# Kernel optimization log

Hardware: AMD Instinct MI355X
Metric: run time of the kernel (lower is better)

Reference implementation:

```python
import jax, jax.numpy as jnp
import numpy as np

EPS_BN = 0.001

def setup_inputs() -> dict:
    key = jax.random.key(0)
    ks = jax.random.split(key, 11)
    B, C, H, W = 32, 512, 64, 64
    Hc = 128
    return {
        'x':  jax.random.normal(ks[0], (B, C, H, W), dtype=jnp.float32),
        'w1': jax.random.normal(ks[1], (Hc, C), dtype=jnp.float32) * (1.0 / np.sqrt(C)),
        'g1': jax.random.uniform(ks[2], (Hc,), dtype=jnp.float32, minval=0.5, maxval=1.5),
        'b1': jax.random.normal(ks[3], (Hc,), dtype=jnp.float32) * 0.1,
        'm1': jax.random.normal(ks[4], (Hc,), dtype=jnp.float32) * 0.1,
        'v1': jax.random.uniform(ks[5], (Hc,), dtype=jnp.float32, minval=0.5, maxval=1.5),
        'w2': jax.random.normal(ks[6], (C, Hc), dtype=jnp.float32) * (1.0 / np.sqrt(Hc)),
        'g2': jax.random.uniform(ks[7], (C,), dtype=jnp.float32, minval=0.5, maxval=1.5),
        'b2': jax.random.normal(ks[8], (C,), dtype=jnp.float32) * 0.1,
        'm2': jax.random.normal(ks[9], (C,), dtype=jnp.float32) * 0.1,
        'v2': jax.random.uniform(ks[10], (C,), dtype=jnp.float32, minval=0.5, maxval=1.5),
    }

def reference(x, w1, g1, b1, m1, v1, w2, g2, b2, m2, v2):
    # squeeze: global average pool -> [B, C]
    s = jnp.mean(x, axis=(2, 3))
    # excitation: 1x1 conv (C->Hc, no bias), eval-mode BN, ReLU, 1x1 conv (Hc->C, no bias)
    h = jnp.einsum('bc,hc->bh', s, w1)
    h = (h - m1) * (g1 * jax.lax.rsqrt(v1 + EPS_BN)) + b1
    h = jax.nn.relu(h)
    e = jnp.einsum('bh,ch->bc', h, w2)  # scale_activation = Identity
    # broadcast scale + final eval-mode BN over channels
    y = x * e[:, :, None, None]
    scale2 = (g2 * jax.lax.rsqrt(v2 + EPS_BN))[None, :, None, None]
    shift2 = (b2 - m2 * g2 * jax.lax.rsqrt(v2 + EPS_BN))[None, :, None, None]
    return y * scale2 + shift2
```

## Files before the change

### kernel.cpp

```cpp
#include <hip/hip_runtime.h>
#include <hip/hip_bf16.h>
#include <stdint.h>

#define B_   32
#define C_   512
#define HW_  4096
#define HC_  128
#define EPS_ 1e-3f

__device__ __forceinline__ float bf_lo(uint32_t u) { return __uint_as_float(u << 16); }
__device__ __forceinline__ float bf_hi(uint32_t u) { return __uint_as_float(u & 0xffff0000u); }

__device__ __forceinline__ uint32_t packbf2(float lo, float hi) {
    union { uint32_t u; __hip_bfloat162 h; } cv;
    cv.h.x = __float2bfloat16(lo);
    cv.h.y = __float2bfloat16(hi);
    return cv.u;
}

__device__ __forceinline__ float ld_scalar(const void* p, int i, int isbf) {
    if (isbf) return __bfloat162float(((const __hip_bfloat16*)p)[i]);
    return ((const float*)p)[i];
}

__global__ __launch_bounds__(256) void se_detect(const uint32_t* __restrict__ v2w,
                                                 int* __restrict__ flag) {
    const int t = threadIdx.x;
    const uint32_t w = v2w[t];
    const float lo = bf_lo(w), hi = bf_hi(w);
    const bool ok = (lo >= 0.4f) && (lo <= 1.6f) && (hi >= 0.4f) && (hi <= 1.6f);
    const unsigned long long bal = __ballot(ok);
    __shared__ int allok[4];
    if ((t & 63) == 0) allok[t >> 6] = (bal == ~0ull) ? 1 : 0;
    __syncthreads();
    if (t == 0) flag[0] = allok[0] & allok[1] & allok[2] & allok[3];
}

__global__ __launch_bounds__(256) void se_pool(const void* __restrict__ x,
                                               float* __restrict__ s,
                                               const int* __restrict__ flag) {
    const int bc = blockIdx.x;
    const int t  = threadIdx.x;
    const int isbf = *flag;
    float sum = 0.f;
    if (isbf) {
        const uint4* p = reinterpret_cast<const uint4*>(x) + (size_t)bc * (HW_ / 8);
        #pragma unroll
        for (int i = t; i < HW_ / 8; i += 256) {
            uint4 v = p[i];
            sum += bf_lo(v.x) + bf_hi(v.x) + bf_lo(v.y) + bf_hi(v.y)
                 + bf_lo(v.z) + bf_hi(v.z) + bf_lo(v.w) + bf_hi(v.w);
        }
    } else {
        const float4* p = reinterpret_cast<const float4*>(x) + (size_t)bc * (HW_ / 4);
        #pragma unroll
        for (int i = t; i < HW_ / 4; i += 256) {
            float4 v = p[i];
            sum += v.x + v.y + v.z + v.w;
        }
    }
    #pragma unroll
    for (int off = 32; off > 0; off >>= 1)
        sum += __shfl_down(sum, off, 64);
    __shared__ float part[4];
    if ((t & 63) == 0) part[t >> 6] = sum;
    __syncthreads();
    if (t == 0) {
        float tot = part[0] + part[1] + part[2] + part[3];
        s[bc] = tot * (1.0f / (float)HW_);
    }
}

__global__ __launch_bounds__(128) void se_excite(
    const float* __restrict__ s,
    const void* __restrict__ w1, const void* __restrict__ g1,
    const void* __restrict__ b1, const void* __restrict__ m1,
    const void* __restrict__ v1, const void* __restrict__ w2,
    const void* __restrict__ g2, const void* __restrict__ b2,
    const void* __restrict__ m2, const void* __restrict__ v2,
    float* __restrict__ A, float* __restrict__ S2,
    const int* __restrict__ flag) {
    __shared__ float s_sh[C_];
    __shared__ float h_sh[HC_];
    const int b = blockIdx.x, t = threadIdx.x;
    const int isbf = *flag;
    for (int i = t; i < C_; i += HC_) s_sh[i] = s[b * C_ + i];
    __syncthreads();

    float acc = 0.f;
    if (isbf) {
        const uint4* w1r = reinterpret_cast<const uint4*>(w1) + (size_t)t * (C_ / 8);
        #pragma unroll 8
        for (int i = 0; i < C_ / 8; ++i) {
            uint4 v = w1r[i];
            const int c = i * 8;
            acc += s_sh[c + 0] * bf_lo(v.x) + s_sh[c + 1] * bf_hi(v.x)
                 + s_sh[c + 2] * bf_lo(v.y) + s_sh[c + 3] * bf_hi(v.y)
                 + s_sh[c + 4] * bf_lo(v.z) + s_sh[c + 5] * bf_hi(v.z)
                 + s_sh[c + 6] * bf_lo(v.w) + s_sh[c + 7] * bf_hi(v.w);
        }
    } else {
        const float4* w1r = reinterpret_cast<const float4*>(w1) + (size_t)t * (C_ / 4);
        #pragma unroll 8
        for (int i = 0; i < C_ / 4; ++i) {
            float4 v = w1r[i];
            const int c = i * 4;
            acc += s_sh[c + 0] * v.x + s_sh[c + 1] * v.y
                 + s_sh[c + 2] * v.z + s_sh[c + 3] * v.w;
        }
    }
    const float sc1 = ld_scalar(g1, t, isbf) * rsqrtf(ld_scalar(v1, t, isbf) + EPS_);
    const float hv  = (acc - ld_scalar(m1, t, isbf)) * sc1 + ld_scalar(b1, t, isbf);
    h_sh[t] = fmaxf(hv, 0.f);
    __syncthreads();

    #pragma unroll
    for (int k = 0; k < C_ / HC_; ++k) {
        const int c = t + HC_ * k;
        float e = 0.f;
        if (isbf) {
            const uint4* w2r = reinterpret_cast<const uint4*>(w2) + (size_t)c * (HC_ / 8);
            #pragma unroll
            for (int i = 0; i < HC_ / 8; ++i) {
                uint4 v = w2r[i];
                const int j = i * 8;
                e += h_sh[j + 0] * bf_lo(v.x) + h_sh[j + 1] * bf_hi(v.x)
                   + h_sh[j + 2] * bf_lo(v.y) + h_sh[j + 3] * bf_hi(v.y)
                   + h_sh[j + 4] * bf_lo(v.z) + h_sh[j + 5] * bf_hi(v.z)
                   + h_sh[j + 6] * bf_lo(v.w) + h_sh[j + 7] * bf_hi(v.w);
            }
        } else {
            const float4* w2r = reinterpret_cast<const float4*>(w2) + (size_t)c * (HC_ / 4);
            #pragma unroll
            for (int i = 0; i < HC_ / 4; ++i) {
                float4 v = w2r[i];
                const int j = i * 4;
                e += h_sh[j + 0] * v.x + h_sh[j + 1] * v.y
                   + h_sh[j + 2] * v.z + h_sh[j + 3] * v.w;
            }
        }
        const float sc2 = ld_scalar(g2, c, isbf) * rsqrtf(ld_scalar(v2, c, isbf) + EPS_);
        A[b * C_ + c] = e * sc2;
        if (b == 0) S2[c] = ld_scalar(b2, c, isbf) - ld_scalar(m2, c, isbf) * sc2;
    }
}

__global__ __launch_bounds__(256) void se_apply(const void* __restrict__ x,
                                                const float* __restrict__ A,
                                                const float* __restrict__ S2,
                                                void* __restrict__ y,
                                                const int* __restrict__ flag) {
    const int bc = blockIdx.x;
    const int t  = threadIdx.x;
    const int isbf = *flag;
    const float a  = A[bc];
    const float sh = S2[bc & (C_ - 1)];
    if (isbf) {
        const uint4* px = reinterpret_cast<const uint4*>(x) + (size_t)bc * (HW_ / 8);
        uint4*       py = reinterpret_cast<uint4*>(y)       + (size_t)bc * (HW_ / 8);
        #pragma unroll
        for (int i = t; i < HW_ / 8; i += 256) {
            uint4 v = px[i];
            uint4 r;
            r.x = packbf2(fmaf(bf_lo(v.x), a, sh), fmaf(bf_hi(v.x), a, sh));
            r.y = packbf2(fmaf(bf_lo(v.y), a, sh), fmaf(bf_hi(v.y), a, sh));
            r.z = packbf2(fmaf(bf_lo(v.z), a, sh), fmaf(bf_hi(v.z), a, sh));
            r.w = packbf2(fmaf(bf_lo(v.w), a, sh), fmaf(bf_hi(v.w), a, sh));
            py[i] = r;
        }
    } else {
        const float4* px = reinterpret_cast<const float4*>(x) + (size_t)bc * (HW_ / 4);
        float4*       py = reinterpret_cast<float4*>(y)       + (size_t)bc * (HW_ / 4);
        #pragma unroll
        for (int i = t; i < HW_ / 4; i += 256) {
            float4 v = px[i];
            float4 r;
            r.x = fmaf(v.x, a, sh);
            r.y = fmaf(v.y, a, sh);
            r.z = fmaf(v.z, a, sh);
            r.w = fmaf(v.w, a, sh);
            py[i] = r;
        }
    }
}

extern "C" void kernel_launch(void* const* d_in, const int* in_sizes, int n_in,
                              void* d_out, int out_size, void* d_ws, size_t ws_size,
                              hipStream_t stream) {
    const void* x  = d_in[0];
    const void* w1 = d_in[1];
    const void* g1 = d_in[2];
    const void* b1 = d_in[3];
    const void* m1 = d_in[4];
    const void* v1 = d_in[5];
    const void* w2 = d_in[6];
    const void* g2 = d_in[7];
    const void* b2 = d_in[8];
    const void* m2 = d_in[9];
    const void* v2 = d_in[10];

    float* ws = (float*)d_ws;
    float* s  = ws;
    float* A  = ws + B_ * C_;
    float* S2 = ws + 2 * B_ * C_;
    int* flag = (int*)(ws + 2 * B_ * C_ + C_);

    se_detect<<<1, 256, 0, stream>>>((const uint32_t*)v2, flag);
    se_pool<<<B_ * C_, 256, 0, stream>>>(x, s, flag);
    se_excite<<<B_, HC_, 0, stream>>>(s, w1, g1, b1, m1, v1, w2, g2, b2, m2, v2,
                                      A, S2, flag);
    se_apply<<<B_ * C_, 256, 0, stream>>>(x, A, S2, d_out, flag);
}
```

Baseline: 524.4 us.

## Inline dtype detection, reverse apply block order, use nontemporal output stores

Removes the separate detect kernel launch by having every block of pool, excite and apply re-derive the bf16/fp32 flag from v2 in shared memory. The apply kernel walks blocks in reverse order so the most recently pooled slices of x, likely still in L2/MALL cache, are re-read first. Output writes become nontemporal stores to avoid polluting cache. Each block now does an extra small global read and two barriers.

```diff
diff --git a/kernel.cpp b/kernel.cpp
--- a/kernel.cpp
+++ b/kernel.cpp
@@ -8,6 +8,9 @@
 #define HC_  128
 #define EPS_ 1e-3f
 
+typedef uint32_t u32x4 __attribute__((ext_vector_type(4)));
+typedef float    f32x4 __attribute__((ext_vector_type(4)));
+
 __device__ __forceinline__ float bf_lo(uint32_t u) { return __uint_as_float(u << 16); }
 __device__ __forceinline__ float bf_hi(uint32_t u) { return __uint_as_float(u & 0xffff0000u); }
 
@@ -23,46 +26,51 @@
     return ((const float*)p)[i];
 }
 
-__global__ __launch_bounds__(256) void se_detect(const uint32_t* __restrict__ v2w,
-                                                 int* __restrict__ flag) {
-    const int t = threadIdx.x;
-    const uint32_t w = v2w[t];
-    const float lo = bf_lo(w), hi = bf_hi(w);
-    const bool ok = (lo >= 0.4f) && (lo <= 1.6f) && (hi >= 0.4f) && (hi <= 1.6f);
-    const unsigned long long bal = __ballot(ok);
-    __shared__ int allok[4];
-    if ((t & 63) == 0) allok[t >> 6] = (bal == ~0ull) ? 1 : 0;
-    __syncthreads();
-    if (t == 0) flag[0] = allok[0] & allok[1] & allok[2] & allok[3];
+template <int NT>
+__device__ __forceinline__ int detect_isbf(const uint32_t* __restrict__ v2w,
+                                           int t, int* s_flag) {
+    if (t == 0) *s_flag = 1;
+    __syncthreads();
+    bool ok = true;
+    #pragma unroll
+    for (int i = t; i < 256; i += NT) {
+        const uint32_t w = v2w[i];
+        const float lo = bf_lo(w), hi = bf_hi(w);
+        ok = ok && (lo >= 0.4f) && (lo <= 1.6f) && (hi >= 0.4f) && (hi <= 1.6f);
+    }
+    if (!ok) *s_flag = 0;
+    __syncthreads();
+    return *s_flag;
 }
 
 __global__ __launch_bounds__(256) void se_pool(const void* __restrict__ x,
                                                float* __restrict__ s,
-                                               const int* __restrict__ flag) {
+                                               const uint32_t* __restrict__ v2w) {
+    __shared__ int s_flag;
+    __shared__ float part[4];
+    const int t  = threadIdx.x;
+    const int isbf = detect_isbf<256>(v2w, t, &s_flag);
     const int bc = blockIdx.x;
-    const int t  = threadIdx.x;
-    const int isbf = *flag;
     float sum = 0.f;
     if (isbf) {
-        const uint4* p = reinterpret_cast<const uint4*>(x) + (size_t)bc * (HW_ / 8);
+        const u32x4* p = reinterpret_cast<const u32x4*>(x) + (size_t)bc * (HW_ / 8);
         #pragma unroll
         for (int i = t; i < HW_ / 8; i += 256) {
-            uint4 v = p[i];
+            u32x4 v = p[i];
             sum += bf_lo(v.x) + bf_hi(v.x) + bf_lo(v.y) + bf_hi(v.y)
                  + bf_lo(v.z) + bf_hi(v.z) + bf_lo(v.w) + bf_hi(v.w);
         }
     } else {
-        const float4* p = reinterpret_cast<const float4*>(x) + (size_t)bc * (HW_ / 4);
+        const f32x4* p = reinterpret_cast<const f32x4*>(x) + (size_t)bc * (HW_ / 4);
         #pragma unroll
         for (int i = t; i < HW_ / 4; i += 256) {
-            float4 v = p[i];
+            f32x4 v = p[i];
             sum += v.x + v.y + v.z + v.w;
         }
     }
     #pragma unroll
     for (int off = 32; off > 0; off >>= 1)
         sum += __shfl_down(sum, off, 64);
-    __shared__ float part[4];
     if ((t & 63) == 0) part[t >> 6] = sum;
     __syncthreads();
     if (t == 0) {
@@ -78,21 +86,21 @@
     const void* __restrict__ v1, const void* __restrict__ w2,
     const void* __restrict__ g2, const void* __restrict__ b2,
     const void* __restrict__ m2, const void* __restrict__ v2,
-    float* __restrict__ A, float* __restrict__ S2,
-    const int* __restrict__ flag) {
+    float* __restrict__ A, float* __restrict__ S2) {
+    __shared__ int s_flag;
     __shared__ float s_sh[C_];
     __shared__ float h_sh[HC_];
     const int b = blockIdx.x, t = threadIdx.x;
-    const int isbf = *flag;
+    const int isbf = detect_isbf<128>((const uint32_t*)v2, t, &s_flag);
     for (int i = t; i < C_; i += HC_) s_sh[i] = s[b * C_ + i];
     __syncthreads();
 
     float acc = 0.f;
     if (isbf) {
-        const uint4* w1r = reinterpret_cast<const uint4*>(w1) + (size_t)t * (C_ / 8);
+        const u32x4* w1r = reinterpret_cast<const u32x4*>(w1) + (size_t)t * (C_ / 8);
         #pragma unroll 8
         for (int i = 0; i < C_ / 8; ++i) {
-            uint4 v = w1r[i];
+            u32x4 v = w1r[i];
             const int c = i * 8;
             acc += s_sh[c + 0] * bf_lo(v.x) + s_sh[c + 1] * bf_hi(v.x)
                  + s_sh[c + 2] * bf_lo(v.y) + s_sh[c + 3] * bf_hi(v.y)
@@ -100,10 +108,10 @@
                  + s_sh[c + 6] * bf_lo(v.w) + s_sh[c + 7] * bf_hi(v.w);
         }
     } else {
-        const float4* w1r = reinterpret_cast<const float4*>(w1) + (size_t)t * (C_ / 4);
+        const f32x4* w1r = reinterpret_cast<const f32x4*>(w1) + (size_t)t * (C_ / 4);
         #pragma unroll 8
         for (int i = 0; i < C_ / 4; ++i) {
-            float4 v = w1r[i];
+            f32x4 v = w1r[i];
             const int c = i * 4;
             acc += s_sh[c + 0] * v.x + s_sh[c + 1] * v.y
                  + s_sh[c + 2] * v.z + s_sh[c + 3] * v.w;
@@ -119,10 +127,10 @@
         const int c = t + HC_ * k;
         float e = 0.f;
         if (isbf) {
-            const uint4* w2r = reinterpret_cast<const uint4*>(w2) + (size_t)c * (HC_ / 8);
+            const u32x4* w2r = reinterpret_cast<const u32x4*>(w2) + (size_t)c * (HC_ / 8);
             #pragma unroll
             for (int i = 0; i < HC_ / 8; ++i) {
-                uint4 v = w2r[i];
+                u32x4 v = w2r[i];
                 const int j = i * 8;
                 e += h_sh[j + 0] * bf_lo(v.x) + h_sh[j + 1] * bf_hi(v.x)
                    + h_sh[j + 2] * bf_lo(v.y) + h_sh[j + 3] * bf_hi(v.y)
@@ -130,10 +138,10 @@
                    + h_sh[j + 6] * bf_lo(v.w) + h_sh[j + 7] * bf_hi(v.w);
             }
         } else {
-            const float4* w2r = reinterpret_cast<const float4*>(w2) + (size_t)c * (HC_ / 4);
+            const f32x4* w2r = reinterpret_cast<const f32x4*>(w2) + (size_t)c * (HC_ / 4);
             #pragma unroll
             for (int i = 0; i < HC_ / 4; ++i) {
-                float4 v = w2r[i];
+                f32x4 v = w2r[i];
                 const int j = i * 4;
                 e += h_sh[j + 0] * v.x + h_sh[j + 1] * v.y
                    + h_sh[j + 2] * v.z + h_sh[j + 3] * v.w;
@@ -149,37 +157,38 @@
                                                 const float* __restrict__ A,
                                                 const float* __restrict__ S2,
                                                 void* __restrict__ y,
-                                                const int* __restrict__ flag) {
-    const int bc = blockIdx.x;
+                                                const uint32_t* __restrict__ v2w) {
+    __shared__ int s_flag;
     const int t  = threadIdx.x;
-    const int isbf = *flag;
+    const int isbf = detect_isbf<256>(v2w, t, &s_flag);
+    const int bc = (B_ * C_ - 1) - (int)blockIdx.x;
     const float a  = A[bc];
     const float sh = S2[bc & (C_ - 1)];
     if (isbf) {
-        const uint4* px = reinterpret_cast<const uint4*>(x) + (size_t)bc * (HW_ / 8);
-        uint4*       py = reinterpret_cast<uint4*>(y)       + (size_t)bc * (HW_ / 8);
+        const u32x4* px = reinterpret_cast<const u32x4*>(x) + (size_t)bc * (HW_ / 8);
+        u32x4*       py = reinterpret_cast<u32x4*>(y)       + (size_t)bc * (HW_ / 8);
         #pragma unroll
         for (int i = t; i < HW_ / 8; i += 256) {
-            uint4 v = px[i];
-            uint4 r;
+            u32x4 v = px[i];
+            u32x4 r;
             r.x = packbf2(fmaf(bf_lo(v.x), a, sh), fmaf(bf_hi(v.x), a, sh));
             r.y = packbf2(fmaf(bf_lo(v.y), a, sh), fmaf(bf_hi(v.y), a, sh));
             r.z = packbf2(fmaf(bf_lo(v.z), a, sh), fmaf(bf_hi(v.z), a, sh));
             r.w = packbf2(fmaf(bf_lo(v.w), a, sh), fmaf(bf_hi(v.w), a, sh));
-            py[i] = r;
+            __builtin_nontemporal_store(r, py + i);
         }
     } else {
-        const float4* px = reinterpret_cast<const float4*>(x) + (size_t)bc * (HW_ / 4);
-        float4*       py = reinterpret_cast<float4*>(y)       + (size_t)bc * (HW_ / 4);
+        const f32x4* px = reinterpret_cast<const f32x4*>(x) + (size_t)bc * (HW_ / 4);
+        f32x4*       py = reinterpret_cast<f32x4*>(y)       + (size_t)bc * (HW_ / 4);
         #pragma unroll
         for (int i = t; i < HW_ / 4; i += 256) {
-            float4 v = px[i];
-            float4 r;
+            f32x4 v = px[i];
+            f32x4 r;
             r.x = fmaf(v.x, a, sh);
             r.y = fmaf(v.y, a, sh);
             r.z = fmaf(v.z, a, sh);
             r.w = fmaf(v.w, a, sh);
-            py[i] = r;
+            __builtin_nontemporal_store(r, py + i);
         }
     }
 }
@@ -203,11 +212,9 @@
     float* s  = ws;
     float* A  = ws + B_ * C_;
     float* S2 = ws + 2 * B_ * C_;
-    int* flag = (int*)(ws + 2 * B_ * C_ + C_);
-
-    se_detect<<<1, 256, 0, stream>>>((const uint32_t*)v2, flag);
-    se_pool<<<B_ * C_, 256, 0, stream>>>(x, s, flag);
+
+    se_pool<<<B_ * C_, 256, 0, stream>>>(x, s, (const uint32_t*)v2);
     se_excite<<<B_, HC_, 0, stream>>>(s, w1, g1, b1, m1, v1, w2, g2, b2, m2, v2,
-                                      A, S2, flag);
-    se_apply<<<B_ * C_, 256, 0, stream>>>(x, A, S2, d_out, flag);
-}
+                                      A, S2);
+    se_apply<<<B_ * C_, 256, 0, stream>>>(x, A, S2, d_out, (const uint32_t*)v2);
+}
```

Measured after the change: 523.6 us. No clear change (-0.1%).
